# Performance work log

Hardware: AMD Instinct MI355X
Metric: run time of the kernel (lower is better)

Reference implementation:

```python
import jax, jax.numpy as jnp
import numpy as np

N_NODES = 50000
N_EDGES = 1600000
L = 16  # lifted_dim

def setup_inputs() -> dict:
    key = jax.random.key(0)
    ks = jax.random.split(key, 12)
    M1 = 2 * L          # 32
    M2 = 4 * M1 + 2 * L  # 160
    s = lambda f: 1.0 / np.sqrt(f)
    return {
        "x_s": jax.random.normal(ks[0], (N_NODES, L), jnp.float32),
        "x_t": jax.random.normal(ks[1], (N_NODES, L), jnp.float32),
        "edge_attr": jax.random.normal(ks[2], (N_EDGES, L), jnp.float32),
        "u": jax.random.normal(ks[3], (1, L), jnp.float32),
        "W1a": jax.random.normal(ks[4], (M1, M1), jnp.float32) * s(M1),
        "b1a": jnp.zeros((M1,), jnp.float32),
        "W2a": jax.random.normal(ks[5], (M1, M1), jnp.float32) * s(M1),
        "b2a": jnp.zeros((M1,), jnp.float32),
        "W1b": jax.random.normal(ks[6], (M2, M2), jnp.float32) * s(M2),
        "b1b": jnp.zeros((M2,), jnp.float32),
        "W2b": jax.random.normal(ks[7], (M2, L), jnp.float32) * s(M2),
        "b2b": jnp.zeros((L,), jnp.float32),
        "gamma": jnp.ones((L,), jnp.float32),
        "beta": jnp.zeros((L,), jnp.float32),
        "edge_index": jax.random.randint(ks[8], (2, N_EDGES), 0, N_NODES, jnp.int32),
    }

def _leaky(x, slope):
    return jnp.where(x >= 0, x, slope * x)

def _forward(x_s, x_t, edge_attr, u, W1a, b1a, W2a, b2a, W1b, b1b, W2b, b2b, gamma, beta, edge_index):
    src, tgt = edge_index[0], edge_index[1]
    n = x_s.shape[0]
    # message MLP on gathered neighbor features
    in_msg = jnp.concatenate([x_t[tgt], edge_attr], axis=1)          # [E, 2L]
    h = _leaky(in_msg @ W1a + b1a, 0.1)
    msg = h @ W2a + b2a                                              # [E, 2L]
    # multi-moment segment reduce
    seg = lambda v: jax.ops.segment_sum(v, src, num_segments=n)
    cnt = seg(jnp.ones((msg.shape[0], 1), msg.dtype))
    denom = jnp.maximum(cnt, 1.0)
    mean = seg(msg) / denom                                          # [N, 2L]
    var = _leaky(seg(msg * msg) / denom - mean * mean, 0.01)
    std = jnp.sqrt(var + 1e-6)
    z = (msg - mean[src]) / std[src]                                 # standardized per-edge
    skew = jnp.nan_to_num(seg(z ** 3) / denom, nan=0.0)
    kurt = jnp.nan_to_num(seg(z ** 4) / denom, nan=0.0)
    h_cat = jnp.concatenate([x_s, mean, std, skew, kurt,
                             jnp.broadcast_to(u, (n, u.shape[1]))], axis=-1)  # [N, 10L]
    h2 = _leaky(h_cat @ W1b + b1b, 0.1)
    out = h2 @ W2b + b2b                                             # [N, L]
    # BatchNorm1d (training-mode batch stats, eps=1e-5)
    mu = jnp.mean(out, axis=0)
    vb = jnp.mean((out - mu) ** 2, axis=0)
    return gamma * (out - mu) * jax.lax.rsqrt(vb + 1e-5) + beta

def reference(x_s, x_t, edge_attr, u, W1a, b1a, W2a, b2a, W1b, b1b, W2b, b2b, gamma, beta, edge_index):
    return _forward(x_s, x_t, edge_attr, u, W1a, b1a, W2a, b2a, W1b, b1b, W2b, b2b, gamma, beta, edge_index)
```

## Files before the change

kernel.cpp:

```cpp
#include <hip/hip_runtime.h>

#define N_NODES 50000
#define N_EDGES 1600000

#define EPB 8192
#define NB1 ((N_EDGES + EPB - 1) / EPB)
#define NPB 128
#define NBK ((N_NODES + NPB - 1) / NPB)
#define TBL (NBK * NB1)
#define NSB ((TBL + 255) / 256)
#define MAXB 4608
#define SCATB 1024
#define NFT 512

typedef unsigned short ushort_t;
typedef __attribute__((ext_vector_type(8))) __bf16 bf16x8;
typedef __attribute__((ext_vector_type(4))) float  f32x4;

union FU { ushort_t s[8]; bf16x8 v; };

__device__ __forceinline__ ushort_t f2bf(float f) {
    union { float f; unsigned int i; } v; v.f = f;
    unsigned int r = v.i + 0x7fffu + ((v.i >> 16) & 1u);
    return (ushort_t)(r >> 16);
}
__device__ __forceinline__ float leaky(float x, float s) { return x >= 0.f ? x : s * x; }

__global__ __launch_bounds__(SCATB) void k_bcount(const int* __restrict__ src, int* __restrict__ table,
                                                  const float* __restrict__ x_t, ushort_t* __restrict__ x_tb) {
    __shared__ int cnt[NBK];
    const int t = threadIdx.x, blk = blockIdx.x;
    const int g = blk * SCATB + t;
    if (g < (N_NODES * 16) / 4) {
        f32x4 v = ((const f32x4*)x_t)[g];
        unsigned long long p = (unsigned long long)f2bf(v[0])
                             | ((unsigned long long)f2bf(v[1]) << 16)
                             | ((unsigned long long)f2bf(v[2]) << 32)
                             | ((unsigned long long)f2bf(v[3]) << 48);
        ((unsigned long long*)x_tb)[g] = p;
    }
    for (int i = t; i < NBK; i += SCATB) cnt[i] = 0;
    __syncthreads();
    const int base = blk * EPB;
    for (int i = t; i < EPB; i += SCATB) {
        int e = base + i;
        if (e < N_EDGES) atomicAdd(&cnt[src[e] >> 7], 1);
    }
    __syncthreads();
    for (int b = t; b < NBK; b += SCATB) table[b * NB1 + blk] = cnt[b];
}

__global__ __launch_bounds__(256) void k_scan1(int* __restrict__ table, int* __restrict__ bsum) {
    __shared__ int buf[256];
    const int t = threadIdx.x, i = blockIdx.x * 256 + t;
    int v = (i < TBL) ? table[i] : 0;
    buf[t] = v; __syncthreads();
    for (int off = 1; off < 256; off <<= 1) {
        int x = (t >= off) ? buf[t - off] : 0;
        __syncthreads(); buf[t] += x; __syncthreads();
    }
    int incl = buf[t];
    if (i < TBL) table[i] = incl - v;
    if (t == 255) bsum[blockIdx.x] = incl;
}
__global__ __launch_bounds__(256) void k_scan2(int* __restrict__ bsum, float* __restrict__ bnsum) {
    __shared__ int sums[256];
    const int t = threadIdx.x;
    if (t < 32) bnsum[t] = 0.f;
    const int SEG = (NSB + 255) / 256;
    const int s0 = t * SEG, s1 = (s0 + SEG < NSB) ? s0 + SEG : NSB;
    int sum = 0;
    for (int i = s0; i < s1; i++) sum += bsum[i];
    sums[t] = sum; __syncthreads();
    for (int off = 1; off < 256; off <<= 1) {
        int x = (t >= off) ? sums[t - off] : 0;
        __syncthreads(); sums[t] += x; __syncthreads();
    }
    int carry = sums[t] - sum;
    for (int i = s0; i < s1; i++) { int v = bsum[i]; bsum[i] = carry; carry += v; }
}

__global__ __launch_bounds__(SCATB) void k_bscat(const int* __restrict__ src, const int* __restrict__ tgt,
                                                 const float* __restrict__ ea, const int* __restrict__ table,
                                                 const int* __restrict__ bsum,
                                                 int* __restrict__ tnA, ushort_t* __restrict__ eaA) {
    __shared__ int cur[NBK];
    const int t = threadIdx.x, blk = blockIdx.x;
    for (int i = t; i < NBK; i += SCATB) {
        int idx = i * NB1 + blk;
        cur[i] = table[idx] + bsum[idx >> 8];
    }
    __syncthreads();
    const int base = blk * EPB;
    for (int i = t; i < EPB; i += SCATB) {
        int e = base + i;
        if (e < N_EDGES) {
            int s = src[e];
            int pos = atomicAdd(&cur[s >> 7], 1);
            tnA[pos] = tgt[e] | ((s & (NPB - 1)) << 16);
            const f32x4* ep = (const f32x4*)(ea + (size_t)e * 16);
            f32x4 v0 = __builtin_nontemporal_load(ep);
            f32x4 v1 = __builtin_nontemporal_load(ep + 1);
            f32x4 v2 = __builtin_nontemporal_load(ep + 2);
            f32x4 v3 = __builtin_nontemporal_load(ep + 3);
            FU lo, hi;
            #pragma unroll
            for (int j = 0; j < 4; j++) {
                lo.s[j] = f2bf(v0[j]); lo.s[4 + j] = f2bf(v1[j]);
                hi.s[j] = f2bf(v2[j]); hi.s[4 + j] = f2bf(v3[j]);
            }
            *(bf16x8*)(eaA + (size_t)pos * 16)     = lo.v;
            *(bf16x8*)(eaA + (size_t)pos * 16 + 8) = hi.v;
        }
    }
}

__global__ __launch_bounds__(NFT) void k_nodeF(
    const ushort_t* __restrict__ x_tb, const ushort_t* __restrict__ eaA, const int* __restrict__ tnA,
    const int* __restrict__ table, const int* __restrict__ bsum,
    const float* __restrict__ w1a, const float* __restrict__ b1a,
    const float* __restrict__ w2a, const float* __restrict__ b2a,
    const float* __restrict__ x_s, const float* __restrict__ u,
    ushort_t* __restrict__ hcat)
{
    __shared__ ushort_t permL[MAXB];
    __shared__ ushort_t tgL[MAXB];
    __shared__ int cntL[NPB], scanL[NPB], curL[NPB];
    __shared__ __align__(16) float h_lds[8][16][36];
    __shared__ ushort_t stat_lds[8][128];

    const int t = threadIdx.x;
    const int w = t >> 6, L = t & 63, q = L >> 4, c = L & 15;
    const int b = blockIdx.x;
    const int i0   = b * NB1;
    const int base = table[i0] + bsum[i0 >> 8];
    int end;
    if (b < NBK - 1) { const int i1 = (b + 1) * NB1; end = table[i1] + bsum[i1 >> 8]; }
    else end = N_EDGES;
    const int cntB0 = end - base;
    const int cntB  = cntB0 < MAXB ? cntB0 : MAXB;

    if (t < NPB) cntL[t] = 0;
    __syncthreads();
    for (int i = t; i < cntB; i += NFT) {
        int v = tnA[base + i];
        tgL[i] = (ushort_t)(v & 0xFFFF);
        atomicAdd(&cntL[v >> 16], 1);
    }
    __syncthreads();
    if (t == 0) {
        int s = 0;
        for (int nl = 0; nl < NPB; nl++) { scanL[nl] = s; s += cntL[nl]; }
    }
    __syncthreads();
    if (t < NPB) curL[t] = scanL[t];
    __syncthreads();
    for (int i = t; i < cntB; i += NFT) {
        int nl = tnA[base + i] >> 16;
        int loc = atomicAdd(&curL[nl], 1);
        permL[loc] = (ushort_t)i;
    }

    bf16x8 B1[2], B2[2];
    #pragma unroll
    for (int h = 0; h < 2; h++) {
        FU u1, u2;
        #pragma unroll
        for (int j = 0; j < 8; j++) {
            int kk = q * 8 + j, nn = c + 16 * h;
            u1.s[j] = f2bf(w1a[kk * 32 + nn]);
            u2.s[j] = f2bf(w2a[kk * 32 + nn]);
        }
        B1[h] = u1.v; B2[h] = u2.v;
    }
    const float bias1[2] = { b1a[c], b1a[c + 16] };
    const float bias2[2] = { b2a[c], b2a[c + 16] };
    const f32x4 zero = { 0.f, 0.f, 0.f, 0.f };
    __syncthreads();

    for (int kn = 0; kn < 16; kn++) {
        const int nl = w * 16 + kn;
        const int n  = b * NPB + nl;
        const int startL = scanL[nl], d = cntL[nl];
        float s1a = 0.f, s2a = 0.f, s3a = 0.f, s4a = 0.f;
        float s1b = 0.f, s2b = 0.f, s3b = 0.f, s4b = 0.f;
        const int ntl = (d + 15) >> 4;

        for (int tl = 0; tl < ntl; tl++) {
            int row  = tl * 16 + c;
            int ridx = row < d ? row : d - 1;
            int li   = permL[startL + ridx];
            FU af;
            if (q < 2) {
                int tg = tgL[li];
                __builtin_memcpy(&af.v, x_tb + (size_t)tg * 16 + q * 8, 16);
            } else {
                __builtin_memcpy(&af.v, eaA + (size_t)(base + li) * 16 + (q - 2) * 8, 16);
            }

            f32x4 a0 = __builtin_amdgcn_mfma_f32_16x16x32_bf16(af.v, B1[0], zero, 0, 0, 0);
            f32x4 a1 = __builtin_amdgcn_mfma_f32_16x16x32_bf16(af.v, B1[1], zero, 0, 0, 0);
            #pragma unroll
            for (int r = 0; r < 4; r++) {
                h_lds[w][q * 4 + r][c]      = leaky(a0[r] + bias1[0], 0.1f);
                h_lds[w][q * 4 + r][c + 16] = leaky(a1[r] + bias1[1], 0.1f);
            }
            __asm__ volatile("s_waitcnt lgkmcnt(0)" ::: "memory");

            float hv[8];
            __builtin_memcpy(&hv, &h_lds[w][c][q * 8], 32);
            FU hf;
            #pragma unroll
            for (int j = 0; j < 8; j++) hf.s[j] = f2bf(hv[j]);
            f32x4 m0 = __builtin_amdgcn_mfma_f32_16x16x32_bf16(hf.v, B2[0], zero, 0, 0, 0);
            f32x4 m1 = __builtin_amdgcn_mfma_f32_16x16x32_bf16(hf.v, B2[1], zero, 0, 0, 0);

            int rb = tl * 16 + q * 4;
            #pragma unroll
            for (int r = 0; r < 4; r++) {
                if (rb + r < d) {
                    float m = m0[r] + bias2[0], mm = m * m;
                    s1a += m;  s2a += mm; s3a += mm * m; s4a += mm * mm;
                    float x = m1[r] + bias2[1], xx = x * x;
                    s1b += x;  s2b += xx; s3b += xx * x; s4b += xx * xx;
                }
            }
        }

        if (n >= N_NODES) continue;

        s1a += __shfl_xor(s1a, 16); s1a += __shfl_xor(s1a, 32);
        s2a += __shfl_xor(s2a, 16); s2a += __shfl_xor(s2a, 32);
        s3a += __shfl_xor(s3a, 16); s3a += __shfl_xor(s3a, 32);
        s4a += __shfl_xor(s4a, 16); s4a += __shfl_xor(s4a, 32);
        s1b += __shfl_xor(s1b, 16); s1b += __shfl_xor(s1b, 32);
        s2b += __shfl_xor(s2b, 16); s2b += __shfl_xor(s2b, 32);
        s3b += __shfl_xor(s3b, 16); s3b += __shfl_xor(s3b, 32);
        s4b += __shfl_xor(s4b, 16); s4b += __shfl_xor(s4b, 32);

        if (q == 0) {
            float denom = fmaxf((float)d, 1.f);
            {
                float mean = s1a / denom, m2r = s2a / denom, m3r = s3a / denom, m4r = s4a / denom;
                float var  = leaky(m2r - mean * mean, 0.01f);
                float stdv = sqrtf(var + 1e-6f);
                float e3   = m3r - 3.f * mean * m2r + 2.f * mean * mean * mean;
                float skew = e3 / (stdv * stdv * stdv);
                float e4   = m4r - 4.f * mean * m3r + 6.f * mean * mean * m2r
                             - 3.f * mean * mean * mean * mean;
                float kurt = e4 / (stdv * stdv * stdv * stdv);
                stat_lds[w][c]      = f2bf(mean);
                stat_lds[w][32 + c] = f2bf(stdv);
                stat_lds[w][64 + c] = f2bf(skew);
                stat_lds[w][96 + c] = f2bf(kurt);
            }
            {
                float mean = s1b / denom, m2r = s2b / denom, m3r = s3b / denom, m4r = s4b / denom;
                float var  = leaky(m2r - mean * mean, 0.01f);
                float stdv = sqrtf(var + 1e-6f);
                float e3   = m3r - 3.f * mean * m2r + 2.f * mean * mean * mean;
                float skew = e3 / (stdv * stdv * stdv);
                float e4   = m4r - 4.f * mean * m3r + 6.f * mean * mean * m2r
                             - 3.f * mean * mean * mean * mean;
                float kurt = e4 / (stdv * stdv * stdv * stdv);
                stat_lds[w][16 + c]  = f2bf(mean);
                stat_lds[w][48 + c]  = f2bf(stdv);
                stat_lds[w][80 + c]  = f2bf(skew);
                stat_lds[w][112 + c] = f2bf(kurt);
            }
        }
        __asm__ volatile("s_waitcnt lgkmcnt(0)" ::: "memory");

        const size_t basep = (size_t)n * 160;
        unsigned int sv;
        __builtin_memcpy(&sv, &stat_lds[w][L * 2], 4);
        *(unsigned int*)(hcat + basep + 16 + L * 2) = sv;
        if (L < 16) {
            hcat[basep + L]       = f2bf(x_s[(size_t)n * 16 + L]);
            hcat[basep + 144 + L] = f2bf(u[L]);
        }
    }
}

__global__ __launch_bounds__(256) void k_gemm1(const ushort_t* __restrict__ hcat,
                                               const float* __restrict__ w1b,
                                               const float* __restrict__ b1b,
                                               ushort_t* __restrict__ h2)
{
    __shared__ __align__(16) ushort_t W1T[160 * 168];
    int t = threadIdx.x;
    for (int i = t; i < 160 * 160; i += 256) { int k = i / 160, n = i % 160; W1T[n * 168 + k] = f2bf(w1b[i]); }
    __syncthreads();
    int w = t >> 6, L = t & 63, q = L >> 4, c = L & 15;
    const f32x4 zero = { 0.f, 0.f, 0.f, 0.f };
    for (int tile = blockIdx.x * 4 + w; tile < 3125 * 10; tile += gridDim.x * 4) {
        int rt = tile / 10, nt = tile % 10;
        int m = rt * 16 + c, n = nt * 16 + c;
        f32x4 acc = zero;
        #pragma unroll
        for (int ks = 0; ks < 5; ks++) {
            bf16x8 a; __builtin_memcpy(&a, hcat + (size_t)m * 160 + ks * 32 + q * 8, 16);
            bf16x8 b; __builtin_memcpy(&b, &W1T[n * 168 + ks * 32 + q * 8], 16);
            acc = __builtin_amdgcn_mfma_f32_16x16x32_bf16(a, b, acc, 0, 0, 0);
        }
        float bias = b1b[n];
        #pragma unroll
        for (int r = 0; r < 4; r++) {
            h2[(size_t)(rt * 16 + q * 4 + r) * 160 + n] = f2bf(leaky(acc[r] + bias, 0.1f));
        }
    }
}

__global__ __launch_bounds__(256) void k_gemm2(const ushort_t* __restrict__ h2,
                                               const float* __restrict__ w2b,
                                               const float* __restrict__ b2b,
                                               float* __restrict__ outpre, float* __restrict__ bnsum)
{
    __shared__ __align__(16) ushort_t W2T[16 * 168];
    int t = threadIdx.x;
    for (int i = t; i < 160 * 16; i += 256) { int k = i / 16, n = i % 16; W2T[n * 168 + k] = f2bf(w2b[i]); }
    __syncthreads();
    int w = t >> 6, L = t & 63, q = L >> 4, c = L & 15;
    const f32x4 zero = { 0.f, 0.f, 0.f, 0.f };
    float ps = 0.f, ps2 = 0.f;
    float bias = b2b[c];
    for (int rt = blockIdx.x * 4 + w; rt < 3125; rt += gridDim.x * 4) {
        int m = rt * 16 + c;
        f32x4 acc = zero;
        #pragma unroll
        for (int ks = 0; ks < 5; ks++) {
            bf16x8 a; __builtin_memcpy(&a, h2 + (size_t)m * 160 + ks * 32 + q * 8, 16);
            bf16x8 b; __builtin_memcpy(&b, &W2T[c * 168 + ks * 32 + q * 8], 16);
            acc = __builtin_amdgcn_mfma_f32_16x16x32_bf16(a, b, acc, 0, 0, 0);
        }
        #pragma unroll
        for (int r = 0; r < 4; r++) {
            float v = acc[r] + bias;
            outpre[(size_t)(rt * 16 + q * 4 + r) * 16 + c] = v;
            ps += v; ps2 += v * v;
        }
    }
    ps  += __shfl_xor(ps, 16);  ps  += __shfl_xor(ps, 32);
    ps2 += __shfl_xor(ps2, 16); ps2 += __shfl_xor(ps2, 32);
    if (q == 0) {
        unsafeAtomicAdd(&bnsum[c], ps);
        unsafeAtomicAdd(&bnsum[16 + c], ps2);
    }
}

__global__ __launch_bounds__(256) void k_bn(const float* __restrict__ outpre, const float* __restrict__ bnsum,
                                            const float* __restrict__ gamma, const float* __restrict__ beta,
                                            float* __restrict__ out)
{
    int i = blockIdx.x * 256 + threadIdx.x;
    int c = i & 15;
    float x = outpre[i];
    float mu = bnsum[c] * (1.f / N_NODES);
    float var = bnsum[16 + c] * (1.f / N_NODES) - mu * mu;
    out[i] = gamma[c] * (x - mu) * rsqrtf(var + 1e-5f) + beta[c];
}

extern "C" void kernel_launch(void* const* d_in, const int* in_sizes, int n_in,
                              void* d_out, int out_size, void* d_ws, size_t ws_size,
                              hipStream_t stream) {
    const float* x_s  = (const float*)d_in[0];
    const float* x_t  = (const float*)d_in[1];
    const float* ea   = (const float*)d_in[2];
    const float* u    = (const float*)d_in[3];
    const float* w1a  = (const float*)d_in[4];
    const float* b1a  = (const float*)d_in[5];
    const float* w2a  = (const float*)d_in[6];
    const float* b2a  = (const float*)d_in[7];
    const float* w1b  = (const float*)d_in[8];
    const float* b1b  = (const float*)d_in[9];
    const float* w2b  = (const float*)d_in[10];
    const float* b2b  = (const float*)d_in[11];
    const float* gam  = (const float*)d_in[12];
    const float* bet  = (const float*)d_in[13];
    const int* eidx   = (const int*)d_in[14];
    const int* src = eidx;
    const int* tgt = eidx + N_EDGES;

    char* ws = (char*)d_ws;
    const size_t OFF_TABLE  = 0;
    const size_t OFF_BSUM   = 614400;
    const size_t OFF_BNSUM  = 655360;
    const size_t OFF_OUTPRE = 786432;
    const size_t OFF_XTB    = 4194304;
    const size_t OFF_TNA    = 6291456;
    const size_t OFF_EAA    = 16777216;
    const size_t OFF_HCAT   = 68157440;
    const size_t OFF_H2     = 84934656;

    int*      table  = (int*)(ws + OFF_TABLE);
    int*      bsum   = (int*)(ws + OFF_BSUM);
    float*    bnsum  = (float*)(ws + OFF_BNSUM);
    float*    outpre = (float*)(ws + OFF_OUTPRE);
    ushort_t* x_tb   = (ushort_t*)(ws + OFF_XTB);
    int*      tnA    = (int*)(ws + OFF_TNA);
    ushort_t* eaA    = (ushort_t*)(ws + OFF_EAA);
    ushort_t* hcat   = (ushort_t*)(ws + OFF_HCAT);
    ushort_t* h2     = (ushort_t*)(ws + OFF_H2);

    k_bcount<<<NB1, SCATB, 0, stream>>>(src, table, x_t, x_tb);
    k_scan1 <<<NSB, 256, 0, stream>>>(table, bsum);
    k_scan2 <<<1,   256, 0, stream>>>(bsum, bnsum);
    k_bscat <<<NB1, SCATB, 0, stream>>>(src, tgt, ea, table, bsum, tnA, eaA);
    k_nodeF <<<NBK, NFT, 0, stream>>>(x_tb, eaA, tnA, table, bsum, w1a, b1a, w2a, b2a, x_s, u, hcat);
    k_gemm1 <<<1024, 256, 0, stream>>>(hcat, w1b, b1b, h2);
    k_gemm2 <<<512,  256, 0, stream>>>(h2, w2b, b2b, outpre, bnsum);
    k_bn    <<<(N_NODES * 16) / 256, 256, 0, stream>>>(outpre, bnsum, gam, bet, (float*)d_out);
}
```

Measured before the change: 415.5 us.

## Stage bucketed edge records in LDS before coalesced global scatter

The bucket scatter kernel now processes each block's edges in sub-chunks of 2048. For each sub-chunk it counts per-bucket occurrences, prefix-scans them in shared memory, and writes the converted bf16 edge attributes into an LDS staging buffer ordered by bucket. A second pass then copies the staged records to global memory, so consecutive threads write to contiguous positions within a bucket instead of random ones. The cost is extra LDS use (about 64KB of staging), several block-wide scans and barriers per sub-chunk, and lower occupancy.

```diff
diff --git a/kernel.cpp b/kernel.cpp
--- a/kernel.cpp
+++ b/kernel.cpp
@@ -12,6 +12,8 @@
 #define MAXB 4608
 #define SCATB 1024
 #define NFT 512
+#define SUBP 2048
+#define NSUB (EPB / SUBP)
 
 typedef unsigned short ushort_t;
 typedef __attribute__((ext_vector_type(8))) __bf16 bf16x8;
@@ -84,20 +86,46 @@
                                                  const float* __restrict__ ea, const int* __restrict__ table,
                                                  const int* __restrict__ bsum,
                                                  int* __restrict__ tnA, ushort_t* __restrict__ eaA) {
-    __shared__ int cur[NBK];
+    __shared__ int curG[NBK];
+    __shared__ int cntL[NBK];
+    __shared__ int curL[NBK];
+    __shared__ int scanS[512];
+    __shared__ ushort_t bucketL[SUBP];
+    __shared__ __align__(16) ushort_t recbuf[SUBP * 16];
+
     const int t = threadIdx.x, blk = blockIdx.x;
     for (int i = t; i < NBK; i += SCATB) {
         int idx = i * NB1 + blk;
-        cur[i] = table[idx] + bsum[idx >> 8];
-    }
-    __syncthreads();
-    const int base = blk * EPB;
-    for (int i = t; i < EPB; i += SCATB) {
-        int e = base + i;
-        if (e < N_EDGES) {
+        curG[i] = table[idx] + bsum[idx >> 8];
+        cntL[i] = 0; curL[i] = 0;
+    }
+    __syncthreads();
+    const int cbase = blk * EPB;
+
+    for (int sp = 0; sp < NSUB; sp++) {
+        const int sbase = cbase + sp * SUBP;
+        const int m = (N_EDGES - sbase < SUBP) ? (N_EDGES - sbase) : SUBP;
+
+        for (int i = t; i < m; i += SCATB) atomicAdd(&cntL[src[sbase + i] >> 7], 1);
+        __syncthreads();
+        if (t < 512) scanS[t] = (t < NBK) ? cntL[t] : 0;
+        __syncthreads();
+        for (int off = 1; off < 512; off <<= 1) {
+            int x = (t < 512 && t >= off) ? scanS[t - off] : 0;
+            __syncthreads();
+            if (t < 512) scanS[t] += x;
+            __syncthreads();
+        }
+        if (t < NBK) scanS[t] -= cntL[t];
+        __syncthreads();
+        for (int i = t; i < m; i += SCATB) {
+            int e = sbase + i;
             int s = src[e];
-            int pos = atomicAdd(&cur[s >> 7], 1);
-            tnA[pos] = tgt[e] | ((s & (NPB - 1)) << 16);
+            int b = s >> 7;
+            int loc = scanS[b] + atomicAdd(&curL[b], 1);
+            bucketL[loc] = (ushort_t)b;
+            int gpos = curG[b] + (loc - scanS[b]);
+            tnA[gpos] = tgt[e] | ((s & (NPB - 1)) << 16);
             const f32x4* ep = (const f32x4*)(ea + (size_t)e * 16);
             f32x4 v0 = __builtin_nontemporal_load(ep);
             f32x4 v1 = __builtin_nontemporal_load(ep + 1);
@@ -109,9 +137,24 @@
                 lo.s[j] = f2bf(v0[j]); lo.s[4 + j] = f2bf(v1[j]);
                 hi.s[j] = f2bf(v2[j]); hi.s[4 + j] = f2bf(v3[j]);
             }
-            *(bf16x8*)(eaA + (size_t)pos * 16)     = lo.v;
-            *(bf16x8*)(eaA + (size_t)pos * 16 + 8) = hi.v;
-        }
+            *(bf16x8*)(recbuf + loc * 16)     = lo.v;
+            *(bf16x8*)(recbuf + loc * 16 + 8) = hi.v;
+        }
+        __syncthreads();
+        for (int loc = t; loc < m; loc += SCATB) {
+            int b = bucketL[loc];
+            int gpos = curG[b] + (loc - scanS[b]);
+            bf16x8 lo = *(bf16x8*)(recbuf + loc * 16);
+            bf16x8 hi = *(bf16x8*)(recbuf + loc * 16 + 8);
+            *(bf16x8*)(eaA + (size_t)gpos * 16)     = lo;
+            *(bf16x8*)(eaA + (size_t)gpos * 16 + 8) = hi;
+        }
+        __syncthreads();
+        for (int i = t; i < NBK; i += SCATB) {
+            curG[i] += cntL[i];
+            cntL[i] = 0; curL[i] = 0;
+        }
+        __syncthreads();
     }
 }
 
```

Result: faster. 404.2 us (-2.7%).
